# Optimization experiments

Measured on AMD Instinct MI355X. Metric: run time of the kernel, lower is better.

The kernel has to match this reference:

```python
import jax, jax.numpy as jnp
import numpy as np

W, H = 256, 256          # image width (x) and height (y); image indexed [x, y] like the torch code
N = 8192                 # depth-sorted visible gaussians
TILE = 16                # tile_size default
CHUNK = 128              # gaussians composited per scan step (N % CHUNK == 0)
MIN_WEIGHT = 1e-6        # early-termination threshold from render_pixel


def setup_inputs() -> dict:
    key = jax.random.key(0)
    k1, k2, k3, k4, k5 = jax.random.split(key, 5)
    # pixel-space means, uniformly over the image
    points_xy = jax.random.uniform(k1, (N, 2), dtype=jnp.float32) * jnp.array([W, H], jnp.float32)
    # SPD inverse 2D covariances: Sigma = R diag(var) R^T, inv = R diag(1/var) R^T
    theta = jax.random.uniform(k2, (N,), dtype=jnp.float32) * (2.0 * np.pi)
    sig = jax.random.uniform(k3, (N, 2), dtype=jnp.float32, minval=1.5, maxval=8.0)
    var = sig ** 2
    ct, st = jnp.cos(theta), jnp.sin(theta)
    R = jnp.stack([jnp.stack([ct, -st], -1), jnp.stack([st, ct], -1)], -2)  # [N,2,2]
    inverse_covariance = jnp.einsum('nij,nj,nkj->nik', R, 1.0 / var, R)
    # radius = ceil(2.5 * sqrt(max eigenvalue)) as in compute_radius
    radius = jnp.ceil(2.5 * jnp.sqrt(jnp.max(var, axis=1)))
    colors = jax.random.uniform(k4, (N, 3), dtype=jnp.float32)
    opacity = jax.random.normal(k5, (N,), dtype=jnp.float32)  # pre-sigmoid logits
    return dict(points_xy=points_xy, inverse_covariance=inverse_covariance,
                radius=radius, colors=colors, opacity=opacity)


def _rasterize(points_xy, inverse_covariance, radius, colors, opacity):
    px = jnp.arange(W, dtype=jnp.float32)[:, None]   # [W,1] pixel x coords
    py = jnp.arange(H, dtype=jnp.float32)[None, :]   # [1,H] pixel y coords
    # tile origin for each pixel (tile-based culling as in render_image)
    tile_x0 = ((jnp.arange(W) // TILE) * TILE).astype(jnp.float32)[:, None]  # [W,1]
    tile_y0 = ((jnp.arange(H) // TILE) * TILE).astype(jnp.float32)[None, :]  # [1,H]
    # per-gaussian bounding boxes (preprocess)
    min_x = jnp.floor(points_xy[:, 0] - radius); max_x = jnp.ceil(points_xy[:, 0] + radius)
    min_y = jnp.floor(points_xy[:, 1] - radius); max_y = jnp.ceil(points_xy[:, 1] + radius)

    n_chunks = N // CHUNK
    def chunk(a):
        return a.reshape((n_chunks, CHUNK) + a.shape[1:])
    xs = dict(mx=chunk(points_xy[:, 0]), my=chunk(points_xy[:, 1]),
              a=chunk(inverse_covariance[:, 0, 0]), b=chunk(inverse_covariance[:, 0, 1]),
              c=chunk(inverse_covariance[:, 1, 1]),
              mnx=chunk(min_x), mxx=chunk(max_x), mny=chunk(min_y), mxy=chunk(max_y),
              col=chunk(colors), op=chunk(opacity))

    @jax.checkpoint
    def body(carry, ch):
        T, color = carry  # T: [W,H] remaining transmittance; color: [W,H,3]
        dx = px[None] - ch['mx'][:, None, None]  # [C,W,1]
        dy = py[None] - ch['my'][:, None, None]  # [C,1,H]
        # mahalanobis form d^T Sigma^{-1} d with symmetric inv cov [[a,b],[b,c]]
        q = (ch['a'][:, None, None] * dx * dx
             + 2.0 * ch['b'][:, None, None] * dx * dy
             + ch['c'][:, None, None] * dy * dy)              # [C,W,H]
        alpha = jnp.exp(-0.5 * q) * jax.nn.sigmoid(ch['op'])[:, None, None]
        # gaussian participates for a pixel iff its bbox intersects that pixel's tile
        in_tile = ((ch['mnx'][:, None, None] <= tile_x0[None] + TILE)
                   & (ch['mxx'][:, None, None] >= tile_x0[None])
                   & (ch['mny'][:, None, None] <= tile_y0[None] + TILE)
                   & (ch['mxy'][:, None, None] >= tile_y0[None]))   # [C,W,H]
        alpha = jnp.where(in_tile, alpha, 0.0)
        cum = jnp.cumprod(1.0 - alpha, axis=0)                 # inclusive prefix of (1-alpha)
        T_before = T[None] * jnp.concatenate([jnp.ones_like(cum[:1]), cum[:-1]], axis=0)
        # original: test_weight = T_before*(1-alpha); terminate (skip contribution) if < min_weight
        include = (T[None] * cum) >= MIN_WEIGHT
        contrib = jnp.where(include, T_before * alpha, 0.0)   # [C,W,H]
        color = color + jnp.einsum('cwh,cd->whd', contrib, ch['col'])
        return (T * cum[-1], color), None

    init = (jnp.ones((W, H), jnp.float32), jnp.zeros((W, H, 3), jnp.float32))
    (_, color), _ = jax.lax.scan(body, init, xs)
    return color  # [W,H,3] image indexed [x,y]


def reference(points_xy, inverse_covariance, radius, colors, opacity):
    return _rasterize(points_xy, inverse_covariance, radius, colors, opacity)
```

## Files before the change

kernel.cpp:

```cpp
#include <hip/hip_runtime.h>
#include <hip/hip_fp16.h>

#define WIDTH   256
#define HEIGHT  256
#define NG      8192
#define TILE_SZ 16
#define MINW    1e-6f
#define BLK     1024
#define NBATCH  (NG / BLK)
#define NWAVE   (BLK / 64)
#define NSEG    4
#define SEGSZ   64
#define ROUND   (NSEG * SEGSZ)

__global__ __launch_bounds__(BLK) void raster_kernel(
    const float* __restrict__ pts,
    const float* __restrict__ icov,
    const float* __restrict__ rad,
    const float* __restrict__ cols,
    const float* __restrict__ opac,
    float* __restrict__ out)
{
    __shared__ unsigned long long s_ball[NBATCH * NWAVE];
    __shared__ int s_pfx[NBATCH * NWAVE];
    __shared__ unsigned short s_list[NG];
    __shared__ float4 s_g[ROUND * 2];
    __shared__ float s_P[NSEG][256];
    __shared__ float s_red[NSEG][256][3];

    const int tid  = threadIdx.x;
    const int lane = tid & 63;
    const int wave = tid >> 6;
    const int seg  = tid >> 8;
    const int px   = tid & 255;
    const float tx0 = (float)(blockIdx.x * TILE_SZ);
    const float ty0 = (float)(blockIdx.y * TILE_SZ);
    const float tx1 = tx0 + (float)TILE_SZ;
    const float ty1 = ty0 + (float)TILE_SZ;

    unsigned int hitbits = 0;
    for (int b = 0; b < NBATCH; ++b) {
        const int g = b * BLK + tid;
        const float2 p = ((const float2*)pts)[g];
        const float  r = rad[g];
        bool hit = (floorf(p.x - r) <= tx1) & (ceilf(p.x + r) >= tx0)
                 & (floorf(p.y - r) <= ty1) & (ceilf(p.y + r) >= ty0);
        unsigned long long m = __ballot(hit);
        if (lane == 0) s_ball[b * NWAVE + wave] = m;
        if (hit) hitbits |= (1u << b);
    }
    __syncthreads();
    if (wave == 0) {
        int v0 = __popcll(s_ball[lane]);
        int v1 = __popcll(s_ball[64 + lane]);
        #pragma unroll
        for (int d = 1; d < 64; d <<= 1) {
            const int t0 = __shfl_up(v0, d);
            const int t1 = __shfl_up(v1, d);
            if (lane >= d) { v0 += t0; v1 += t1; }
        }
        s_pfx[lane] = v0;
        s_pfx[64 + lane] = v1 + __shfl(v0, 63);
    }
    __syncthreads();
    const int count = s_pfx[127];
    {
        unsigned int hb = hitbits;
        const unsigned long long ltmask = (1ull << lane) - 1ull;
        while (hb) {
            const int b = __ffs(hb) - 1;  hb &= hb - 1;
            const int idx = b * NWAVE + wave;
            const unsigned long long m = s_ball[idx];
            const int bs = idx ? s_pfx[idx - 1] : 0;
            s_list[bs + __popcll(m & ltmask)] = (unsigned short)(b * BLK + tid);
        }
    }
    __syncthreads();

    const float fx = tx0 + (float)(px >> 4);
    const float fy = ty0 + (float)(px & 15);
    const float kc = -0.72134752044f;
    float T = 1.0f, accr = 0.0f, accg = 0.0f, accb = 0.0f;
    const int s0 = seg * SEGSZ;

    for (int base = 0; base < count; base += ROUND) {
        const int n = min(ROUND, count - base);
        if (tid < ROUND) {
            float4 w0 = make_float4(0.f, 0.f, 0.f, 0.f);
            float4 w1 = make_float4(0.f, 0.f, 0.f, 0.f);
            if (tid < n) {
                const int g = s_list[base + tid];
                const float2 p = ((const float2*)pts)[g];
                const float4 ic = ((const float4*)icov)[g];
                const float op = 1.0f / (1.0f + __expf(-opac[g]));
                const __half2 h = __floats2half2_rn(cols[3 * g], cols[3 * g + 1]);
                unsigned rgbits; __builtin_memcpy(&rgbits, &h, 4);
                w0 = make_float4(p.x, p.y, kc * ic.x, 2.0f * kc * ic.y);
                w1 = make_float4(kc * ic.w, op, __uint_as_float(rgbits), cols[3 * g + 2]);
            }
            s_g[tid * 2 + 0] = w0;
            s_g[tid * 2 + 1] = w1;
        }
        __syncthreads();

        float P = 1.0f, lr = 0.0f, lg = 0.0f, lb = 0.0f;
        if (__ballot(T >= MINW) != 0ull) {
            #pragma unroll 8
            for (int i = 0; i < SEGSZ; ++i) {
                const int idx = s0 + i;
                const float4 g0 = s_g[idx * 2 + 0];
                const float4 g1 = s_g[idx * 2 + 1];
                const float dx = fx - g0.x, dy = fy - g0.y;
                const float q = (g0.z * dx) * dx + (g0.w * dx) * dy + (g1.x * dy) * dy;
                const float a = g1.y * __builtin_amdgcn_exp2f(q);
                const float w = P * a;
                const unsigned rgbits = __float_as_uint(g1.z);
                __half2 h; __builtin_memcpy(&h, &rgbits, 4);
                const float2 rg = __half22float2(h);
                lr = fmaf(w, rg.x, lr);
                lg = fmaf(w, rg.y, lg);
                lb = fmaf(w, g1.w, lb);
                P *= (1.0f - a);
            }
        }
        s_P[seg][px] = P;
        __syncthreads();

        const float p0 = s_P[0][px], p1 = s_P[1][px], p2 = s_P[2][px], p3 = s_P[3][px];
        float Tin = T;
        if (seg > 0) Tin *= p0;
        if (seg > 1) Tin *= p1;
        if (seg > 2) Tin *= p2;
        const float Tnext = (((T * p0) * p1) * p2) * p3;

        const bool alive = (Tin >= MINW);
        const bool gated = alive && (Tin * P < MINW);
        if (alive && !gated) {
            accr = fmaf(Tin, lr, accr);
            accg = fmaf(Tin, lg, accg);
            accb = fmaf(Tin, lb, accb);
        }
        if (__ballot(gated) != 0ull) {
            float Tl = Tin;
            #pragma unroll 4
            for (int i = 0; i < SEGSZ; ++i) {
                const int idx = s0 + i;
                const float4 g0 = s_g[idx * 2 + 0];
                const float4 g1 = s_g[idx * 2 + 1];
                const float dx = fx - g0.x, dy = fy - g0.y;
                const float q = (g0.z * dx) * dx + (g0.w * dx) * dy + (g1.x * dy) * dy;
                const float a = g1.y * __builtin_amdgcn_exp2f(q);
                const float Tn = Tl * (1.0f - a);
                const float w = (gated && Tn >= MINW) ? Tl * a : 0.0f;
                const unsigned rgbits = __float_as_uint(g1.z);
                __half2 h; __builtin_memcpy(&h, &rgbits, 4);
                const float2 rg = __half22float2(h);
                accr = fmaf(w, rg.x, accr);
                accg = fmaf(w, rg.y, accg);
                accb = fmaf(w, g1.w, accb);
                Tl = Tn;
            }
        }
        T = Tnext;
        if (__syncthreads_count(T < MINW) == BLK) break;
    }

    s_red[seg][px][0] = accr;
    s_red[seg][px][1] = accg;
    s_red[seg][px][2] = accb;
    __syncthreads();
    if (tid < 256) {
        const float r = s_red[0][tid][0] + s_red[1][tid][0] + s_red[2][tid][0] + s_red[3][tid][0];
        const float g = s_red[0][tid][1] + s_red[1][tid][1] + s_red[2][tid][1] + s_red[3][tid][1];
        const float b = s_red[0][tid][2] + s_red[1][tid][2] + s_red[2][tid][2] + s_red[3][tid][2];
        const int x = blockIdx.x * TILE_SZ + (tid >> 4);
        const int y = blockIdx.y * TILE_SZ + (tid & 15);
        const int o = (x * HEIGHT + y) * 3;
        out[o] = r;  out[o + 1] = g;  out[o + 2] = b;
    }
}

extern "C" void kernel_launch(void* const* d_in, const int* in_sizes, int n_in,
                              void* d_out, int out_size, void* d_ws, size_t ws_size,
                              hipStream_t stream) {
    const float* pts  = (const float*)d_in[0];
    const float* icov = (const float*)d_in[1];
    const float* rad  = (const float*)d_in[2];
    const float* cols = (const float*)d_in[3];
    const float* opac = (const float*)d_in[4];
    float* out = (float*)d_out;
    dim3 grid(WIDTH / TILE_SZ, HEIGHT / TILE_SZ);
    raster_kernel<<<grid, dim3(BLK), 0, stream>>>(pts, icov, rad, cols, opac, out);
}
```

Baseline: 92.70 us.

## Split each tile across two blocks with eight gaussian segments per round

Each 16x16 tile is now handled by two blocks (grid z=2) of 128 pixels each, and the 1024 threads are split into eight segments rather than four. Each round stages up to 1024 gaussians, and every segment composites a contiguous slice of them before the segments' transmittance products are combined. This doubles the block count to fill more CUs and shortens the serial per-thread chain, but the tile culling and list build are repeated in both blocks. The larger rounds can also over-process gaussians past the early-termination point, and the final reduction is rewritten to write one channel per thread.

```diff
diff --git a/kernel.cpp b/kernel.cpp
--- a/kernel.cpp
+++ b/kernel.cpp
@@ -9,11 +9,11 @@
 #define BLK     1024
 #define NBATCH  (NG / BLK)
 #define NWAVE   (BLK / 64)
-#define NSEG    4
-#define SEGSZ   64
-#define ROUND   (NSEG * SEGSZ)
+#define NSEG    8
+#define PXB     128
+#define RSZ     1024
 
-__global__ __launch_bounds__(BLK) void raster_kernel(
+__global__ __launch_bounds__(BLK, 8) void raster_kernel(
     const float* __restrict__ pts,
     const float* __restrict__ icov,
     const float* __restrict__ rad,
@@ -24,15 +24,16 @@
     __shared__ unsigned long long s_ball[NBATCH * NWAVE];
     __shared__ int s_pfx[NBATCH * NWAVE];
     __shared__ unsigned short s_list[NG];
-    __shared__ float4 s_g[ROUND * 2];
-    __shared__ float s_P[NSEG][256];
-    __shared__ float s_red[NSEG][256][3];
+    __shared__ float4 s_g[RSZ * 2];
+    __shared__ float s_P[NSEG][PXB];
+    __shared__ float s_red[NSEG][PXB][3];
 
     const int tid  = threadIdx.x;
     const int lane = tid & 63;
     const int wave = tid >> 6;
-    const int seg  = tid >> 8;
-    const int px   = tid & 255;
+    const int seg  = tid >> 7;
+    const int pxl  = tid & (PXB - 1);
+    const int px   = blockIdx.z * PXB + pxl;
     const float tx0 = (float)(blockIdx.x * TILE_SZ);
     const float ty0 = (float)(blockIdx.y * TILE_SZ);
     const float tx1 = tx0 + (float)TILE_SZ;
@@ -81,35 +82,32 @@
     const float fy = ty0 + (float)(px & 15);
     const float kc = -0.72134752044f;
     float T = 1.0f, accr = 0.0f, accg = 0.0f, accb = 0.0f;
-    const int s0 = seg * SEGSZ;
 
-    for (int base = 0; base < count; base += ROUND) {
-        const int n = min(ROUND, count - base);
-        if (tid < ROUND) {
-            float4 w0 = make_float4(0.f, 0.f, 0.f, 0.f);
-            float4 w1 = make_float4(0.f, 0.f, 0.f, 0.f);
-            if (tid < n) {
-                const int g = s_list[base + tid];
-                const float2 p = ((const float2*)pts)[g];
-                const float4 ic = ((const float4*)icov)[g];
-                const float op = 1.0f / (1.0f + __expf(-opac[g]));
-                const __half2 h = __floats2half2_rn(cols[3 * g], cols[3 * g + 1]);
-                unsigned rgbits; __builtin_memcpy(&rgbits, &h, 4);
-                w0 = make_float4(p.x, p.y, kc * ic.x, 2.0f * kc * ic.y);
-                w1 = make_float4(kc * ic.w, op, __uint_as_float(rgbits), cols[3 * g + 2]);
-            }
-            s_g[tid * 2 + 0] = w0;
-            s_g[tid * 2 + 1] = w1;
+    for (int base = 0; base < count; base += RSZ) {
+        const int n = min(RSZ, count - base);
+        if (tid < n) {
+            const int g = s_list[base + tid];
+            const float2 p = ((const float2*)pts)[g];
+            const float4 ic = ((const float4*)icov)[g];
+            const float op = 1.0f / (1.0f + __expf(-opac[g]));
+            const __half2 h = __floats2half2_rn(cols[3 * g], cols[3 * g + 1]);
+            unsigned rgbits; __builtin_memcpy(&rgbits, &h, 4);
+            s_g[tid * 2 + 0] = make_float4(p.x, p.y, kc * ic.x, 2.0f * kc * ic.y);
+            s_g[tid * 2 + 1] = make_float4(kc * ic.w, op, __uint_as_float(rgbits),
+                                           cols[3 * g + 2]);
         }
         __syncthreads();
 
+        const int L = (n + NSEG - 1) >> 3;
+        const int i0 = seg * L;
+        const int i1 = min(i0 + L, n);
+
         float P = 1.0f, lr = 0.0f, lg = 0.0f, lb = 0.0f;
         if (__ballot(T >= MINW) != 0ull) {
-            #pragma unroll 8
-            for (int i = 0; i < SEGSZ; ++i) {
-                const int idx = s0 + i;
-                const float4 g0 = s_g[idx * 2 + 0];
-                const float4 g1 = s_g[idx * 2 + 1];
+            #pragma unroll 4
+            for (int i = i0; i < i1; ++i) {
+                const float4 g0 = s_g[i * 2 + 0];
+                const float4 g1 = s_g[i * 2 + 1];
                 const float dx = fx - g0.x, dy = fy - g0.y;
                 const float q = (g0.z * dx) * dx + (g0.w * dx) * dy + (g1.x * dy) * dy;
                 const float a = g1.y * __builtin_amdgcn_exp2f(q);
@@ -120,18 +118,21 @@
                 lr = fmaf(w, rg.x, lr);
                 lg = fmaf(w, rg.y, lg);
                 lb = fmaf(w, g1.w, lb);
-                P *= (1.0f - a);
+                P = fmaf(-a, P, P);
             }
         }
-        s_P[seg][px] = P;
+        s_P[seg][pxl] = P;
         __syncthreads();
 
-        const float p0 = s_P[0][px], p1 = s_P[1][px], p2 = s_P[2][px], p3 = s_P[3][px];
-        float Tin = T;
-        if (seg > 0) Tin *= p0;
-        if (seg > 1) Tin *= p1;
-        if (seg > 2) Tin *= p2;
-        const float Tnext = (((T * p0) * p1) * p2) * p3;
+        float pv[NSEG];
+        #pragma unroll
+        for (int s = 0; s < NSEG; ++s) pv[s] = s_P[s][pxl];
+        float Tin = T, Tnext = T;
+        #pragma unroll
+        for (int s = 0; s < NSEG; ++s) {
+            if (s < seg) Tin *= pv[s];
+            Tnext *= pv[s];
+        }
 
         const bool alive = (Tin >= MINW);
         const bool gated = alive && (Tin * P < MINW);
@@ -142,11 +143,9 @@
         }
         if (__ballot(gated) != 0ull) {
             float Tl = Tin;
-            #pragma unroll 4
-            for (int i = 0; i < SEGSZ; ++i) {
-                const int idx = s0 + i;
-                const float4 g0 = s_g[idx * 2 + 0];
-                const float4 g1 = s_g[idx * 2 + 1];
+            for (int i = i0; i < i1; ++i) {
+                const float4 g0 = s_g[i * 2 + 0];
+                const float4 g1 = s_g[i * 2 + 1];
                 const float dx = fx - g0.x, dy = fy - g0.y;
                 const float q = (g0.z * dx) * dx + (g0.w * dx) * dy + (g1.x * dy) * dy;
                 const float a = g1.y * __builtin_amdgcn_exp2f(q);
@@ -165,18 +164,20 @@
         if (__syncthreads_count(T < MINW) == BLK) break;
     }
 
-    s_red[seg][px][0] = accr;
-    s_red[seg][px][1] = accg;
-    s_red[seg][px][2] = accb;
+    s_red[seg][pxl][0] = accr;
+    s_red[seg][pxl][1] = accg;
+    s_red[seg][pxl][2] = accb;
     __syncthreads();
-    if (tid < 256) {
-        const float r = s_red[0][tid][0] + s_red[1][tid][0] + s_red[2][tid][0] + s_red[3][tid][0];
-        const float g = s_red[0][tid][1] + s_red[1][tid][1] + s_red[2][tid][1] + s_red[3][tid][1];
-        const float b = s_red[0][tid][2] + s_red[1][tid][2] + s_red[2][tid][2] + s_red[3][tid][2];
-        const int x = blockIdx.x * TILE_SZ + (tid >> 4);
-        const int y = blockIdx.y * TILE_SZ + (tid & 15);
-        const int o = (x * HEIGHT + y) * 3;
-        out[o] = r;  out[o + 1] = g;  out[o + 2] = b;
+    if (tid < PXB * 3) {
+        const int p  = tid / 3;
+        const int ch = tid - 3 * p;
+        float v = 0.0f;
+        #pragma unroll
+        for (int s = 0; s < NSEG; ++s) v += s_red[s][p][ch];
+        const int pg = blockIdx.z * PXB + p;
+        const int x = blockIdx.x * TILE_SZ + (pg >> 4);
+        const int y = blockIdx.y * TILE_SZ + (pg & 15);
+        out[(x * HEIGHT + y) * 3 + ch] = v;
     }
 }
 
@@ -189,6 +190,6 @@
     const float* cols = (const float*)d_in[3];
     const float* opac = (const float*)d_in[4];
     float* out = (float*)d_out;
-    dim3 grid(WIDTH / TILE_SZ, HEIGHT / TILE_SZ);
+    dim3 grid(WIDTH / TILE_SZ, HEIGHT / TILE_SZ, 2);
     raster_kernel<<<grid, dim3(BLK), 0, stream>>>(pts, icov, rad, cols, opac, out);
 }
```

After: 84.82 us. 1.09x faster.
